# Performance work log

Measured on AMD Instinct MI355X. Metric: run time of the kernel, lower is better.

The kernel has to match this reference:

```python
import jax, jax.numpy as jnp
import numpy as np

B, H, N, D = 16, 8, 256, 32


def setup_inputs() -> dict:
    key = jax.random.key(0)
    k1, k2, k3 = jax.random.split(key, 3)
    q = jax.random.normal(k1, (B, H, N, D), dtype=jnp.float32)
    k = jax.random.normal(k2, (B, H, N, D), dtype=jnp.float32)
    scale = jnp.ones((1,), dtype=jnp.float32)  # unused by the module
    mask = jnp.zeros((B, 1, N, N), dtype=bool)  # True == masked out
    # learned attention vector, xavier_uniform over (1, H, 1, 1, D)
    fan = 1 * H * 1 * 1 * D
    bound = float(np.sqrt(6.0 / (1 + D)))  # xavier for (..., D) param
    attention = jax.random.uniform(k3, (1, H, 1, 1, D), dtype=jnp.float32,
                                   minval=-bound, maxval=bound)
    return {"q": q, "k": k, "scale": scale, "mask": mask, "attention": attention}


def reference(q, k, scale, mask, attention):
    # summed: [B, H, Nq, Nk, D] via broadcast of q.unsqueeze(-2)+k.unsqueeze(-3)
    summed = q[:, :, :, None, :] + k[:, :, None, :, :]
    # GATv2 score: a^T * silu(q_i + k_j), reduced over head_dim
    scores = jnp.sum(jax.nn.silu(summed) * attention, axis=-1)  # [B, H, Nq, Nk]
    neg = jnp.finfo(scores.dtype).min
    scores_masked = jnp.where(mask, neg, scores)
    attn = jax.nn.softmax(scores_masked, axis=-1)
    return attn
```

## Files before the change

kernel.cpp:

```cpp
#include <hip/hip_runtime.h>
#include <stdint.h>
#include <stddef.h>

constexpr int Bc = 16, Hc = 8, Nc = 256, Dc = 32;
constexpr float LOG2E = 1.44269504088896340736f;

constexpr int    MF    = 10;
constexpr double PHALF = 9.7;
constexpr double LFIT  = 9.0;

constexpr double PI_ = 3.14159265358979323846;

constexpr double cexp_(double x) {
    int n = (int)(x >= 0 ? x + 0.5 : x - 0.5);
    double f = x - n, t = 1.0, s = 1.0;
    for (int i = 1; i <= 26; ++i) { t *= f / i; s += t; }
    const double E = 2.71828182845904523536;
    double en = 1.0, bb = n >= 0 ? E : 1.0 / E;
    int an = n < 0 ? -n : n;
    for (int i = 0; i < an; ++i) en *= bb;
    return s * en;
}
constexpr double creduce_(double x) {
    while (x >  PI_) x -= 2.0 * PI_;
    while (x < -PI_) x += 2.0 * PI_;
    return x;
}
constexpr double ccos_(double x0) {
    double x = creduce_(x0), x2 = x * x, t = 1.0, s = 1.0;
    for (int i = 1; i <= 16; ++i) { t *= -x2 / ((2.0*i - 1.0) * (2.0*i)); s += t; }
    return s;
}
constexpr double csin_(double x0) {
    double x = creduce_(x0), x2 = x * x, t = x, s = x;
    for (int i = 1; i <= 16; ++i) { t *= -x2 / ((2.0*i) * (2.0*i + 1.0)); s += t; }
    return s;
}
constexpr double Gfun_(double x) {
    double z = x < 0 ? -x : x;
    double e = cexp_(z);
    return 0.5 * z * ((e - 1.0) / (e + 1.0));
}
constexpr double csqrt_(double x) {
    if (x <= 0) return 0;
    double r = x > 1 ? x : 1;
    for (int i = 0; i < 40; ++i) r = 0.5 * (r + x / r);
    return r;
}

struct FitT { float tk[MF + 1]; float tq[MF + 1]; };

constexpr FitT lsFit_() {
    constexpr int NB = MF + 1;
    double A[NB][NB] = {}, bv[NB] = {};
    for (int p = 0; p < NB; ++p)
        for (int qq = 0; qq < NB; ++qq) {
            double wm = (p - qq) * PI_ / PHALF, wp = (p + qq) * PI_ / PHALF;
            double Sm = (p == qq)     ? LFIT : csin_(wm * LFIT) / wm;
            double Sp = (p + qq == 0) ? LFIT : csin_(wp * LFIT) / wp;
            A[p][qq] = 0.5 * (Sm + Sp);
        }
    constexpr int NS = 128;
    double hh = LFIT / NS, gx[NS + 1] = {};
    for (int i = 0; i <= NS; ++i) gx[i] = Gfun_(i * hh);
    for (int p = 0; p < NB; ++p) {
        double s = 0;
        for (int i = 0; i <= NS; ++i) {
            double wgt = (i == 0 || i == NS) ? 1.0 : ((i & 1) ? 4.0 : 2.0);
            s += wgt * gx[i] * ccos_(p * PI_ / PHALF * (i * hh));
        }
        bv[p] = s * hh / 3.0;
    }
    for (int p = 0; p < NB; ++p) A[p][p] += 1e-8 * LFIT;
    for (int col = 0; col < NB; ++col) {
        int piv = col; double best = A[col][col] < 0 ? -A[col][col] : A[col][col];
        for (int r = col + 1; r < NB; ++r) {
            double v = A[r][col] < 0 ? -A[r][col] : A[r][col];
            if (v > best) { best = v; piv = r; }
        }
        if (piv != col) {
            for (int cc = 0; cc < NB; ++cc) { double t = A[col][cc]; A[col][cc] = A[piv][cc]; A[piv][cc] = t; }
            double t = bv[col]; bv[col] = bv[piv]; bv[piv] = t;
        }
        for (int r = col + 1; r < NB; ++r) {
            double f = A[r][col] / A[col][col];
            for (int cc = col; cc < NB; ++cc) A[r][cc] -= f * A[col][cc];
            bv[r] -= f * bv[col];
        }
    }
    double c[NB] = {};
    for (int r = NB - 1; r >= 0; --r) {
        double s = bv[r];
        for (int cc = r + 1; cc < NB; ++cc) s -= A[r][cc] * c[cc];
        c[r] = s / A[r][r];
    }
    FitT f{};
    for (int m = 0; m <= MF; ++m) {
        double rt = csqrt_(c[m] < 0 ? -c[m] : c[m]);
        f.tk[m] = (float)rt;
        f.tq[m] = (float)(c[m] < 0 ? -rt : rt);
    }
    return f;
}
constexpr FitT CF = lsFit_();

typedef _Float16 half8  __attribute__((ext_vector_type(8)));
typedef float    f32x16 __attribute__((ext_vector_type(16)));

__device__ __forceinline__ uint32_t pkh_(float a, float b) {
    auto v = __builtin_amdgcn_cvt_pkrtz(a, b);
    uint32_t u; __builtin_memcpy(&u, &v, 4); return u;
}

constexpr int ROWB = 144;
constexpr int KB_  = Nc * ROWB;
constexpr int QB_  = 128 * ROWB;
constexpr int BUF  = KB_ + QB_;
constexpr int SRED_OFF = 2 * BUF;
constexpr int AKV_OFF  = SRED_OFF + 2048;
constexpr int SMEM     = AKV_OFF + 1024;

__global__ __launch_bounds__(1024, 4) void gatv2_mfma_kernel(
    const float* __restrict__ q, const float* __restrict__ k,
    const uint8_t* __restrict__ mask, const float* __restrict__ att,
    float* __restrict__ out)
{
    extern __shared__ char smem[];
    float* sred = (float*)(smem + SRED_OFF);
    float* akv  = (float*)(smem + AKV_OFF);

    const int tid = threadIdx.x, lane = tid & 63, w = tid >> 6;
    const int bh = blockIdx.y, h = bh & 7, b = bh >> 3;
    const int iBlk = blockIdx.x * 128;
    const float invTwoP = (float)(1.0 / (2.0 * PHALF));

    if (w >= 8) {
        const int p = tid - 512, dq = p & 7, rw = p >> 3;
        const float4 a4p = *(const float4*)(att + h * Dc + 4 * dq);
        float kc1[16], ks1[16], kcm[16], ksm[16];
        float qc1[8], qs1[8], qcm[8], qsm[8];
        int offK[4], offQ[2];

        const float* kbase = k + (size_t)bh * Nc * Dc;
#pragma unroll
        for (int it = 0; it < 4; ++it) {
            const int j = rw + it * 64;
            const float4 kv = *(const float4*)(kbase + j * Dc + 4 * dq);
            float part = a4p.x * kv.x + a4p.y * kv.y + a4p.z * kv.z + a4p.w * kv.w;
            part += __shfl_xor(part, 1, 64);
            part += __shfl_xor(part, 2, 64);
            part += __shfl_xor(part, 4, 64);
            if (dq == 0) akv[j] = part;
            const float rv[4] = { kv.x, kv.y, kv.z, kv.w };
#pragma unroll
            for (int c = 0; c < 4; ++c) {
                float r = __builtin_amdgcn_fractf(rv[c] * invTwoP);
                kc1[4*it+c] = __builtin_amdgcn_cosf(r);
                ks1[4*it+c] = __builtin_amdgcn_sinf(r);
                kcm[4*it+c] = kc1[4*it+c];
                ksm[4*it+c] = ks1[4*it+c];
            }
            offK[it] = j * ROWB + dq * 16;
        }
        const float* qbase = q + ((size_t)bh * Nc + iBlk) * Dc;
#pragma unroll
        for (int it = 0; it < 2; ++it) {
            const int iq = rw + it * 64;
            const float4 qv = *(const float4*)(qbase + iq * Dc + 4 * dq);
            const float rv[4] = { qv.x, qv.y, qv.z, qv.w };
#pragma unroll
            for (int c = 0; c < 4; ++c) {
                float r = __builtin_amdgcn_fractf(rv[c] * invTwoP);
                qc1[4*it+c] = __builtin_amdgcn_cosf(r);
                qs1[4*it+c] = __builtin_amdgcn_sinf(r);
                qcm[4*it+c] = qc1[4*it+c];
                qsm[4*it+c] = qs1[4*it+c];
            }
            offQ[it] = KB_ + iq * ROWB + dq * 16;
        }

        auto buildWrite = [&](int mN, int dstOff) {
            const float tk = CF.tk[mN];
            const float g0 = CF.tq[mN]*a4p.x, g1 = CF.tq[mN]*a4p.y;
            const float g2 = CF.tq[mN]*a4p.z, g3 = CF.tq[mN]*a4p.w;
#pragma unroll
            for (int it = 0; it < 4; ++it) {
                uint4 wv;
                wv.x = pkh_(tk * kcm[4*it+0], tk * ksm[4*it+0]);
                wv.y = pkh_(tk * kcm[4*it+1], tk * ksm[4*it+1]);
                wv.z = pkh_(tk * kcm[4*it+2], tk * ksm[4*it+2]);
                wv.w = pkh_(tk * kcm[4*it+3], tk * ksm[4*it+3]);
                *(uint4*)(smem + dstOff + offK[it]) = wv;
            }
#pragma unroll
            for (int it = 0; it < 2; ++it) {
                uint4 wv;
                wv.x = pkh_(g0 * qcm[4*it+0], -(g0 * qsm[4*it+0]));
                wv.y = pkh_(g1 * qcm[4*it+1], -(g1 * qsm[4*it+1]));
                wv.z = pkh_(g2 * qcm[4*it+2], -(g2 * qsm[4*it+2]));
                wv.w = pkh_(g3 * qcm[4*it+3], -(g3 * qsm[4*it+3]));
                *(uint4*)(smem + dstOff + offQ[it]) = wv;
            }
        };
        auto rotate = [&]() {
#pragma unroll
            for (int e = 0; e < 16; ++e) {
                float cn = fmaf(kc1[e], kcm[e], -(ks1[e] * ksm[e]));
                float sn = fmaf(ks1[e], kcm[e],   kc1[e] * ksm[e]);
                kcm[e] = cn; ksm[e] = sn;
            }
#pragma unroll
            for (int e = 0; e < 8; ++e) {
                float cn = fmaf(qc1[e], qcm[e], -(qs1[e] * qsm[e]));
                float sn = fmaf(qs1[e], qcm[e],   qc1[e] * qsm[e]);
                qcm[e] = cn; qsm[e] = sn;
            }
        };

        buildWrite(1, 0);
        rotate();
        __syncthreads();
#pragma unroll
        for (int m = 1; m < MF; ++m) {
            buildWrite(m + 1, (m & 1) * BUF);
            if (m < MF - 1) rotate();
            __syncthreads();
        }
        __syncthreads();
    } else {
        const int hi5 = lane >> 5, col = lane & 31;
        const int wi = w & 1, wj = (w >> 1) & 3;
        const int baseA0 = KB_ + (wi * 64 + col) * ROWB, baseA1 = baseA0 + 32 * ROWB;
        const int baseB0 = (wj * 64 + col) * ROWB,       baseB1 = baseB0 + 32 * ROWB;

        f32x16 acc[2][2];
#pragma unroll
        for (int i2 = 0; i2 < 2; ++i2)
#pragma unroll
            for (int j2 = 0; j2 < 2; ++j2)
#pragma unroll
                for (int e = 0; e < 16; ++e) acc[i2][j2][e] = 0.0f;

        auto loadFrags = [&](int srcOff, int s, half8& A0, half8& A1,
                             half8& B0, half8& B1) {
            const int du = (2 * s + hi5) << 4;
            A0 = *(const half8*)(smem + srcOff + baseA0 + du);
            A1 = *(const half8*)(smem + srcOff + baseA1 + du);
            B0 = *(const half8*)(smem + srcOff + baseB0 + du);
            B1 = *(const half8*)(smem + srcOff + baseB1 + du);
        };
        auto mfma4 = [&](half8 A0, half8 A1, half8 B0, half8 B1) {
            acc[0][0] = __builtin_amdgcn_mfma_f32_32x32x16_f16(A0, B0, acc[0][0], 0, 0, 0);
            acc[0][1] = __builtin_amdgcn_mfma_f32_32x32x16_f16(A0, B1, acc[0][1], 0, 0, 0);
            acc[1][0] = __builtin_amdgcn_mfma_f32_32x32x16_f16(A1, B0, acc[1][0], 0, 0, 0);
            acc[1][1] = __builtin_amdgcn_mfma_f32_32x32x16_f16(A1, B1, acc[1][1], 0, 0, 0);
        };

        __syncthreads();
#pragma unroll
        for (int m = 1; m <= MF; ++m) {
            const int srcOff = ((m - 1) & 1) * BUF;
            half8 A0a, A1a, B0a, B1a, A0b, A1b, B0b, B1b;
            loadFrags(srcOff, 0, A0a, A1a, B0a, B1a);
            loadFrags(srcOff, 1, A0b, A1b, B0b, B1b);
            __builtin_amdgcn_s_setprio(1);
            mfma4(A0a, A1a, B0a, B1a);
            loadFrags(srcOff, 2, A0a, A1a, B0a, B1a);
            mfma4(A0b, A1b, B0b, B1b);
            loadFrags(srcOff, 3, A0b, A1b, B0b, B1b);
            mfma4(A0a, A1a, B0a, B1a);
            mfma4(A0b, A1b, B0b, B1b);
            __builtin_amdgcn_s_setprio(0);
            if (m < MF) __syncthreads();
        }

        constexpr float M0 = 24.0f;
        const int jB = wj * 64;
        const int iB = iBlk + wi * 64;
        const float akj0 = akv[jB + col], akj1 = akv[jB + 32 + col];
#pragma unroll
        for (int i2 = 0; i2 < 2; ++i2) {
            float v[16];
#pragma unroll
            for (int e = 0; e < 16; ++e) {
                const int rloc = (e & 3) + 8 * (e >> 2) + 4 * hi5;
                const int ig = iB + i2 * 32 + rloc;
                const uint8_t* mr = mask + ((size_t)(b * Nc + ig)) * Nc + jB + col;
                const uint8_t m0 = mr[0], m1 = mr[32];
                float v0 = fmaf(0.5f, akj0, acc[i2][0][e]);
                float v1 = fmaf(0.5f, akj1, acc[i2][1][e]);
                float p0 = __builtin_amdgcn_exp2f(__builtin_fminf((v0 - M0) * LOG2E, 80.0f));
                float p1 = __builtin_amdgcn_exp2f(__builtin_fminf((v1 - M0) * LOG2E, 80.0f));
                if (m0) p0 = 0.0f;
                if (m1) p1 = 0.0f;
                acc[i2][0][e] = p0;
                acc[i2][1][e] = p1;
                v[e] = p0 + p1;
            }
            float u8[8];
#pragma unroll
            for (int jj = 0; jj < 8; ++jj) {
                float mn = (col & 16) ? v[jj + 8] : v[jj];
                float sd = (col & 16) ? v[jj]     : v[jj + 8];
                u8[jj] = mn + __shfl_xor(sd, 16, 64);
            }
            float u4[4];
#pragma unroll
            for (int jj = 0; jj < 4; ++jj) {
                float mn = (col & 8) ? u8[jj + 4] : u8[jj];
                float sd = (col & 8) ? u8[jj]     : u8[jj + 4];
                u4[jj] = mn + __shfl_xor(sd, 8, 64);
            }
            float u2[2];
#pragma unroll
            for (int jj = 0; jj < 2; ++jj) {
                float mn = (col & 4) ? u4[jj + 2] : u4[jj];
                float sd = (col & 4) ? u4[jj]     : u4[jj + 2];
                u2[jj] = mn + __shfl_xor(sd, 4, 64);
            }
            float t1;
            {
                float mn = (col & 2) ? u2[1] : u2[0];
                float sd = (col & 2) ? u2[0] : u2[1];
                t1 = mn + __shfl_xor(sd, 2, 64);
            }
            t1 += __shfl_xor(t1, 1, 64);
            {
                const int eL = ((col & 16) ? 8 : 0) + ((col & 8) ? 4 : 0)
                             + ((col & 4) ? 2 : 0) + ((col & 2) ? 1 : 0);
                const int rl = (eL & 3) + 8 * (eL >> 2) + 4 * hi5;
                if (!(col & 1)) sred[(wi * 64 + i2 * 32 + rl) * 4 + wj] = t1;
            }
        }
        __syncthreads();

        float* obase = out + (size_t)bh * Nc * Nc;
#pragma unroll
        for (int i2 = 0; i2 < 2; ++i2)
#pragma unroll
        for (int e = 0; e < 16; ++e) {
            const int rloc = (e & 3) + 8 * (e >> 2) + 4 * hi5;
            const int iL = wi * 64 + i2 * 32 + rloc;
            const int ig = iBlk + iL;
            const float4 tv = *(const float4*)(&sred[iL * 4]);
            const float inv = __builtin_amdgcn_rcpf(tv.x + tv.y + tv.z + tv.w);
            obase[(size_t)ig * Nc + jB + col]      = acc[i2][0][e] * inv;
            obase[(size_t)ig * Nc + jB + 32 + col] = acc[i2][1][e] * inv;
        }
    }
}

extern "C" void kernel_launch(void* const* d_in, const int* in_sizes, int n_in,
                              void* d_out, int out_size, void* d_ws, size_t ws_size,
                              hipStream_t stream) {
    const float*   q    = (const float*)d_in[0];
    const float*   k    = (const float*)d_in[1];
    const uint8_t* mask = (const uint8_t*)d_in[3];
    const float*   att  = (const float*)d_in[4];
    float*         out  = (float*)d_out;

    (void)hipFuncSetAttribute((const void*)gatv2_mfma_kernel,
                              hipFuncAttributeMaxDynamicSharedMemorySize, SMEM);

    dim3 grid(2, Bc * Hc);
    dim3 block(1024);
    gatv2_mfma_kernel<<<grid, block, SMEM, stream>>>(q, k, mask, att, out);
}
```

Before: 90.71 us.

## Halve block size, give each MFMA wave a 64x128 tile and producers double work

Shrinks the block from 1024 to 512 threads, with 4 producer waves building the Fourier feature tiles and 4 consumer waves running MFMA. Each consumer wave now computes a 64x128 output tile with 8 accumulators instead of 64x64, so each A fragment is reused across four B fragments and the softmax row reduction spans only two column groups. This trades more registers per thread and more per-thread producer work (cos/sin rotation and stores) for fewer waves, less LDS fragment traffic per MFMA and a smaller cross-wave reduction. It also risks lower occupancy and less latency hiding.

After: 93.75 us. +3.4%, slower.

```diff
diff --git a/kernel.cpp b/kernel.cpp
--- a/kernel.cpp
+++ b/kernel.cpp
@@ -117,10 +117,10 @@
 constexpr int QB_  = 128 * ROWB;
 constexpr int BUF  = KB_ + QB_;
 constexpr int SRED_OFF = 2 * BUF;
-constexpr int AKV_OFF  = SRED_OFF + 2048;
+constexpr int AKV_OFF  = SRED_OFF + 1024;
 constexpr int SMEM     = AKV_OFF + 1024;
 
-__global__ __launch_bounds__(1024, 4) void gatv2_mfma_kernel(
+__global__ __launch_bounds__(512, 2) void gatv2_mfma_kernel(
     const float* __restrict__ q, const float* __restrict__ k,
     const uint8_t* __restrict__ mask, const float* __restrict__ att,
     float* __restrict__ out)
@@ -134,17 +134,17 @@
     const int iBlk = blockIdx.x * 128;
     const float invTwoP = (float)(1.0 / (2.0 * PHALF));
 
-    if (w >= 8) {
-        const int p = tid - 512, dq = p & 7, rw = p >> 3;
+    if (w >= 4) {
+        const int p = tid - 256, dq = p & 7, rw = p >> 3;
         const float4 a4p = *(const float4*)(att + h * Dc + 4 * dq);
-        float kc1[16], ks1[16], kcm[16], ksm[16];
-        float qc1[8], qs1[8], qcm[8], qsm[8];
-        int offK[4], offQ[2];
+        float kc1[32], ks1[32], kcm[32], ksm[32];
+        float qc1[16], qs1[16], qcm[16], qsm[16];
+        int offK[8], offQ[4];
 
         const float* kbase = k + (size_t)bh * Nc * Dc;
 #pragma unroll
-        for (int it = 0; it < 4; ++it) {
-            const int j = rw + it * 64;
+        for (int it = 0; it < 8; ++it) {
+            const int j = rw + it * 32;
             const float4 kv = *(const float4*)(kbase + j * Dc + 4 * dq);
             float part = a4p.x * kv.x + a4p.y * kv.y + a4p.z * kv.z + a4p.w * kv.w;
             part += __shfl_xor(part, 1, 64);
@@ -164,8 +164,8 @@
         }
         const float* qbase = q + ((size_t)bh * Nc + iBlk) * Dc;
 #pragma unroll
-        for (int it = 0; it < 2; ++it) {
-            const int iq = rw + it * 64;
+        for (int it = 0; it < 4; ++it) {
+            const int iq = rw + it * 32;
             const float4 qv = *(const float4*)(qbase + iq * Dc + 4 * dq);
             const float rv[4] = { qv.x, qv.y, qv.z, qv.w };
 #pragma unroll
@@ -184,7 +184,7 @@
             const float g0 = CF.tq[mN]*a4p.x, g1 = CF.tq[mN]*a4p.y;
             const float g2 = CF.tq[mN]*a4p.z, g3 = CF.tq[mN]*a4p.w;
 #pragma unroll
-            for (int it = 0; it < 4; ++it) {
+            for (int it = 0; it < 8; ++it) {
                 uint4 wv;
                 wv.x = pkh_(tk * kcm[4*it+0], tk * ksm[4*it+0]);
                 wv.y = pkh_(tk * kcm[4*it+1], tk * ksm[4*it+1]);
@@ -193,7 +193,7 @@
                 *(uint4*)(smem + dstOff + offK[it]) = wv;
             }
 #pragma unroll
-            for (int it = 0; it < 2; ++it) {
+            for (int it = 0; it < 4; ++it) {
                 uint4 wv;
                 wv.x = pkh_(g0 * qcm[4*it+0], -(g0 * qsm[4*it+0]));
                 wv.y = pkh_(g1 * qcm[4*it+1], -(g1 * qsm[4*it+1]));
@@ -204,13 +204,13 @@
         };
         auto rotate = [&]() {
 #pragma unroll
-            for (int e = 0; e < 16; ++e) {
+            for (int e = 0; e < 32; ++e) {
                 float cn = fmaf(kc1[e], kcm[e], -(ks1[e] * ksm[e]));
                 float sn = fmaf(ks1[e], kcm[e],   kc1[e] * ksm[e]);
                 kcm[e] = cn; ksm[e] = sn;
             }
 #pragma unroll
-            for (int e = 0; e < 8; ++e) {
+            for (int e = 0; e < 16; ++e) {
                 float cn = fmaf(qc1[e], qcm[e], -(qs1[e] * qsm[e]));
                 float sn = fmaf(qs1[e], qcm[e],   qc1[e] * qsm[e]);
                 qcm[e] = cn; qsm[e] = sn;
@@ -229,55 +229,66 @@
         __syncthreads();
     } else {
         const int hi5 = lane >> 5, col = lane & 31;
-        const int wi = w & 1, wj = (w >> 1) & 3;
+        const int wi = w & 1, wj = (w >> 1) & 1;
         const int baseA0 = KB_ + (wi * 64 + col) * ROWB, baseA1 = baseA0 + 32 * ROWB;
-        const int baseB0 = (wj * 64 + col) * ROWB,       baseB1 = baseB0 + 32 * ROWB;
-
-        f32x16 acc[2][2];
+        const int bB = (wj * 128 + col) * ROWB;
+        const int baseB0 = bB,            baseB1 = bB + 32 * ROWB;
+        const int baseB2 = bB + 64*ROWB,  baseB3 = bB + 96 * ROWB;
+
+        f32x16 acc[2][4];
 #pragma unroll
         for (int i2 = 0; i2 < 2; ++i2)
 #pragma unroll
-            for (int j2 = 0; j2 < 2; ++j2)
-#pragma unroll
-                for (int e = 0; e < 16; ++e) acc[i2][j2][e] = 0.0f;
+            for (int j4 = 0; j4 < 4; ++j4)
+#pragma unroll
+                for (int e = 0; e < 16; ++e) acc[i2][j4][e] = 0.0f;
 
         auto loadFrags = [&](int srcOff, int s, half8& A0, half8& A1,
-                             half8& B0, half8& B1) {
+                             half8& B0, half8& B1, half8& B2, half8& B3) {
             const int du = (2 * s + hi5) << 4;
             A0 = *(const half8*)(smem + srcOff + baseA0 + du);
             A1 = *(const half8*)(smem + srcOff + baseA1 + du);
             B0 = *(const half8*)(smem + srcOff + baseB0 + du);
             B1 = *(const half8*)(smem + srcOff + baseB1 + du);
+            B2 = *(const half8*)(smem + srcOff + baseB2 + du);
+            B3 = *(const half8*)(smem + srcOff + baseB3 + du);
         };
-        auto mfma4 = [&](half8 A0, half8 A1, half8 B0, half8 B1) {
+        auto mfma8 = [&](half8 A0, half8 A1, half8 B0, half8 B1,
+                         half8 B2, half8 B3) {
             acc[0][0] = __builtin_amdgcn_mfma_f32_32x32x16_f16(A0, B0, acc[0][0], 0, 0, 0);
             acc[0][1] = __builtin_amdgcn_mfma_f32_32x32x16_f16(A0, B1, acc[0][1], 0, 0, 0);
+            acc[0][2] = __builtin_amdgcn_mfma_f32_32x32x16_f16(A0, B2, acc[0][2], 0, 0, 0);
+            acc[0][3] = __builtin_amdgcn_mfma_f32_32x32x16_f16(A0, B3, acc[0][3], 0, 0, 0);
             acc[1][0] = __builtin_amdgcn_mfma_f32_32x32x16_f16(A1, B0, acc[1][0], 0, 0, 0);
             acc[1][1] = __builtin_amdgcn_mfma_f32_32x32x16_f16(A1, B1, acc[1][1], 0, 0, 0);
+            acc[1][2] = __builtin_amdgcn_mfma_f32_32x32x16_f16(A1, B2, acc[1][2], 0, 0, 0);
+            acc[1][3] = __builtin_amdgcn_mfma_f32_32x32x16_f16(A1, B3, acc[1][3], 0, 0, 0);
         };
 
         __syncthreads();
 #pragma unroll
         for (int m = 1; m <= MF; ++m) {
             const int srcOff = ((m - 1) & 1) * BUF;
-            half8 A0a, A1a, B0a, B1a, A0b, A1b, B0b, B1b;
-            loadFrags(srcOff, 0, A0a, A1a, B0a, B1a);
-            loadFrags(srcOff, 1, A0b, A1b, B0b, B1b);
+            half8 A0a, A1a, B0a, B1a, B2a, B3a;
+            half8 A0b, A1b, B0b, B1b, B2b, B3b;
+            loadFrags(srcOff, 0, A0a, A1a, B0a, B1a, B2a, B3a);
+            loadFrags(srcOff, 1, A0b, A1b, B0b, B1b, B2b, B3b);
             __builtin_amdgcn_s_setprio(1);
-            mfma4(A0a, A1a, B0a, B1a);
-            loadFrags(srcOff, 2, A0a, A1a, B0a, B1a);
-            mfma4(A0b, A1b, B0b, B1b);
-            loadFrags(srcOff, 3, A0b, A1b, B0b, B1b);
-            mfma4(A0a, A1a, B0a, B1a);
-            mfma4(A0b, A1b, B0b, B1b);
+            mfma8(A0a, A1a, B0a, B1a, B2a, B3a);
+            loadFrags(srcOff, 2, A0a, A1a, B0a, B1a, B2a, B3a);
+            mfma8(A0b, A1b, B0b, B1b, B2b, B3b);
+            loadFrags(srcOff, 3, A0b, A1b, B0b, B1b, B2b, B3b);
+            mfma8(A0a, A1a, B0a, B1a, B2a, B3a);
+            mfma8(A0b, A1b, B0b, B1b, B2b, B3b);
             __builtin_amdgcn_s_setprio(0);
             if (m < MF) __syncthreads();
         }
 
         constexpr float M0 = 24.0f;
-        const int jB = wj * 64;
+        const int jB = wj * 128;
         const int iB = iBlk + wi * 64;
-        const float akj0 = akv[jB + col], akj1 = akv[jB + 32 + col];
+        const float akj0 = akv[jB + col],      akj1 = akv[jB + 32 + col];
+        const float akj2 = akv[jB + 64 + col], akj3 = akv[jB + 96 + col];
 #pragma unroll
         for (int i2 = 0; i2 < 2; ++i2) {
             float v[16];
@@ -286,16 +297,25 @@
                 const int rloc = (e & 3) + 8 * (e >> 2) + 4 * hi5;
                 const int ig = iB + i2 * 32 + rloc;
                 const uint8_t* mr = mask + ((size_t)(b * Nc + ig)) * Nc + jB + col;
-                const uint8_t m0 = mr[0], m1 = mr[32];
+                const uint8_t m0 = mr[0],  m1 = mr[32];
+                const uint8_t m2 = mr[64], m3 = mr[96];
                 float v0 = fmaf(0.5f, akj0, acc[i2][0][e]);
                 float v1 = fmaf(0.5f, akj1, acc[i2][1][e]);
+                float v2 = fmaf(0.5f, akj2, acc[i2][2][e]);
+                float v3 = fmaf(0.5f, akj3, acc[i2][3][e]);
                 float p0 = __builtin_amdgcn_exp2f(__builtin_fminf((v0 - M0) * LOG2E, 80.0f));
                 float p1 = __builtin_amdgcn_exp2f(__builtin_fminf((v1 - M0) * LOG2E, 80.0f));
+                float p2 = __builtin_amdgcn_exp2f(__builtin_fminf((v2 - M0) * LOG2E, 80.0f));
+                float p3 = __builtin_amdgcn_exp2f(__builtin_fminf((v3 - M0) * LOG2E, 80.0f));
                 if (m0) p0 = 0.0f;
                 if (m1) p1 = 0.0f;
+                if (m2) p2 = 0.0f;
+                if (m3) p3 = 0.0f;
                 acc[i2][0][e] = p0;
                 acc[i2][1][e] = p1;
-                v[e] = p0 + p1;
+                acc[i2][2][e] = p2;
+                acc[i2][3][e] = p3;
+                v[e] = (p0 + p1) + (p2 + p3);
             }
             float u8[8];
 #pragma unroll
@@ -329,7 +349,7 @@
                 const int eL = ((col & 16) ? 8 : 0) + ((col & 8) ? 4 : 0)
                              + ((col & 4) ? 2 : 0) + ((col & 2) ? 1 : 0);
                 const int rl = (eL & 3) + 8 * (eL >> 2) + 4 * hi5;
-                if (!(col & 1)) sred[(wi * 64 + i2 * 32 + rl) * 4 + wj] = t1;
+                if (!(col & 1)) sred[(wi * 64 + i2 * 32 + rl) * 2 + wj] = t1;
             }
         }
         __syncthreads();
@@ -342,10 +362,13 @@
             const int rloc = (e & 3) + 8 * (e >> 2) + 4 * hi5;
             const int iL = wi * 64 + i2 * 32 + rloc;
             const int ig = iBlk + iL;
-            const float4 tv = *(const float4*)(&sred[iL * 4]);
-            const float inv = __builtin_amdgcn_rcpf(tv.x + tv.y + tv.z + tv.w);
-            obase[(size_t)ig * Nc + jB + col]      = acc[i2][0][e] * inv;
-            obase[(size_t)ig * Nc + jB + 32 + col] = acc[i2][1][e] * inv;
+            const float2 tv = *(const float2*)(&sred[iL * 2]);
+            const float inv = __builtin_amdgcn_rcpf(tv.x + tv.y);
+            float* orow = obase + (size_t)ig * Nc + jB + col;
+            orow[0]  = acc[i2][0][e] * inv;
+            orow[32] = acc[i2][1][e] * inv;
+            orow[64] = acc[i2][2][e] * inv;
+            orow[96] = acc[i2][3][e] * inv;
         }
     }
 }
@@ -363,6 +386,6 @@
                               hipFuncAttributeMaxDynamicSharedMemorySize, SMEM);
 
     dim3 grid(2, Bc * Hc);
-    dim3 block(1024);
+    dim3 block(512);
     gatv2_mfma_kernel<<<grid, block, SMEM, stream>>>(q, k, mask, att, out);
 }
```
